# Optimization experiments

Hardware: AMD Instinct MI355X
Metric: run time of the kernel (lower is better)

Reference implementation:

```python
import jax, jax.numpy as jnp
import numpy as np

EPS = 1e-6  # F.pairwise_distance eps, added to each coordinate difference


def setup_inputs() -> dict:
    key = jax.random.key(0)
    x = jax.random.normal(key, (8192, 3, 192), dtype=jnp.float32)
    return {"x": x}


def reference(x):
    # x: [N, M, D]; positive = shot 0, anchor = mean of shots 1:
    anchor = jnp.mean(x[:, 1:, :], axis=1)          # [N, D]
    pos = x[:, 0, :]                                # [N, D]
    N, D = pos.shape

    # Legacy pairwise_distance reduces over D of the broadcast [N, D, N] diff:
    # dist2[i, j] = sum_d (pos[i,d] - anchor[j,d] + eps)^2
    # Expand exactly via GEMM to avoid materializing [N, D, N]:
    # = ||pos_i||^2 + ||anc_j||^2 - 2 pos_i.anc_j + 2*eps*(sum_d pos_i - sum_d anc_j) + D*eps^2
    pn = jnp.sum(pos * pos, axis=1)                 # [N]
    an = jnp.sum(anchor * anchor, axis=1)           # [N]
    cross = pos @ anchor.T                          # [N, N]
    sdiff = jnp.sum(pos, axis=1)[:, None] - jnp.sum(anchor, axis=1)[None, :]
    dist2 = pn[:, None] + an[None, :] - 2.0 * cross + 2.0 * EPS * sdiff + D * (EPS * EPS)
    output = -dist2                                 # [N, N] logits

    labels = jnp.arange(N)
    logp = jax.nn.log_softmax(output, axis=-1)
    nloss = -jnp.mean(jnp.take_along_axis(logp, labels[:, None], axis=1))

    pred = jnp.argmax(output, axis=1)               # top-1
    prec1 = jnp.mean((pred == labels).astype(jnp.float32)) * 100.0
    return (nloss, prec1)
```

## Files before the change

kernel.cpp:

```cpp
#include <hip/hip_runtime.h>
#include <math.h>


#define NROWS  8192
#define DDIM   192
#define KSPL   384
#define X3     576
#define FEPS   1e-6f
#define LOG2E  1.4426950408889634f
#define LN2    0.6931471805599453f

#define BM 128
#define BN 128
#define BK 64
#define KSTEPS 6
#define NSPLIT 8
#define JRANGE 1024
#define JTILES 8
#define NPART  16
#define NCOMB  32

typedef _Float16 f16;
typedef _Float16 f16x4 __attribute__((ext_vector_type(4)));
typedef _Float16 f16x8 __attribute__((ext_vector_type(8)));
typedef float    f32x4 __attribute__((ext_vector_type(4)));

__device__ __forceinline__ void async_copy16(const void* g, void* l) {
  __builtin_amdgcn_global_load_lds(
      (const __attribute__((address_space(1))) unsigned int*)g,
      (__attribute__((address_space(3))) unsigned int*)l, 16, 0, 0);
}

__global__ __launch_bounds__(256) void prep_kernel(const float* __restrict__ x,
                                                   f16* __restrict__ ph,
                                                   f16* __restrict__ ah,
                                                   float* __restrict__ bvec) {
  const int row  = (blockIdx.x * 256 + threadIdx.x) >> 6;
  const int lane = threadIdx.x & 63;
  float an = 0.f, as = 0.f;
  if (lane < 48) {
    const float* xr = x + (size_t)row * X3;
    const int d = lane * 4;
    const float4 p = *(const float4*)(xr + d);
    const float4 u = *(const float4*)(xr + DDIM + d);
    const float4 w = *(const float4*)(xr + 2 * DDIM + d);
    const float a0 = 0.5f * (u.x + w.x), a1 = 0.5f * (u.y + w.y);
    const float a2 = 0.5f * (u.z + w.z), a3 = 0.5f * (u.w + w.w);
    an = a0 * a0 + a1 * a1 + a2 * a2 + a3 * a3;
    as = a0 + a1 + a2 + a3;
    const float C2 = 2.0f * LOG2E;
    const float p0 = p.x * C2, p1 = p.y * C2, p2 = p.z * C2, p3 = p.w * C2;
    const f16 h0 = (f16)p0, h1 = (f16)p1, h2 = (f16)p2, h3 = (f16)p3;
    f16x4 hv = {h0, h1, h2, h3};
    f16x4 lv = {(f16)(p0 - (float)h0), (f16)(p1 - (float)h1),
                (f16)(p2 - (float)h2), (f16)(p3 - (float)h3)};
    *(f16x4*)(ph + (size_t)row * KSPL + d) = hv;
    *(f16x4*)(ph + (size_t)row * KSPL + DDIM + d) = lv;
    const f16 g0 = (f16)a0, g1 = (f16)a1, g2 = (f16)a2, g3 = (f16)a3;
    f16x4 gv = {g0, g1, g2, g3};
    f16x4 mv = {(f16)(a0 - (float)g0), (f16)(a1 - (float)g1),
                (f16)(a2 - (float)g2), (f16)(a3 - (float)g3)};
    *(f16x4*)(ah + (size_t)row * KSPL + d) = gv;
    *(f16x4*)(ah + (size_t)row * KSPL + DDIM + d) = mv;
  }
  #pragma unroll
  for (int m = 32; m; m >>= 1) {
    an += __shfl_xor(an, m);
    as += __shfl_xor(as, m);
  }
  if (lane == 0) bvec[row] = LOG2E * (-an + 2.0f * FEPS * as);
}

__global__ __launch_bounds__(256, 2) void main_kernel(
    const f16* __restrict__ Ag, const f16* __restrict__ Bg,
    const float* __restrict__ bvec,
    float* __restrict__ pm, float* __restrict__ ps, int* __restrict__ pa,
    float* __restrict__ diag) {
  __shared__ __align__(16) f16 As[2][BM * BK];
  __shared__ __align__(16) f16 Bs[2][BN * BK];
  const int tid  = threadIdx.x;
  const int lane = tid & 63;
  const int wid  = tid >> 6;
  const int wm = wid >> 1, wn = wid & 1;
  const int lLow = lane & 15, lHi = lane >> 4, l7 = lane & 7;
  const int i0 = blockIdx.x * BM;
  const int split = blockIdx.y;

  const int rsub = lane >> 3;
  const int srck = ((lane & 7) ^ rsub) * 8;

  auto stage = [&](int b, int jt, int kc) {
    const int j0 = split * JRANGE + jt * BN;
    #pragma unroll
    for (int q = 0; q < 4; ++q) {
      const int ci  = q * 4 + wid;
      const int row = ci * 8 + rsub;
      async_copy16(Ag + (size_t)(i0 + row) * KSPL + kc + srck, (void*)(&As[b][ci * 512]));
      async_copy16(Bg + (size_t)(j0 + row) * KSPL + kc + srck, (void*)(&Bs[b][ci * 512]));
    }
  };

  float mrun[16], srun[16];
  int   arun[16];
  #pragma unroll
  for (int r = 0; r < 16; ++r) { mrun[r] = -3.0e38f; srun[r] = 0.f; arun[r] = 0; }

  stage(0, 0, 0);
  __syncthreads();

  for (int jt = 0; jt < JTILES; ++jt) {
    f32x4 acc[4][4];
    #pragma unroll
    for (int mf = 0; mf < 4; ++mf)
      #pragma unroll
      for (int nf = 0; nf < 4; ++nf) acc[mf][nf] = (f32x4)0.f;

    #pragma unroll
    for (int ks = 0; ks < KSTEPS; ++ks) {
      if (!(jt == JTILES - 1 && ks == KSTEPS - 1)) {
        const int jn = (ks == KSTEPS - 1) ? jt + 1 : jt;
        const int kn = (ks == KSTEPS - 1) ? 0 : (ks + 1) * BK;
        stage((ks + 1) & 1, jn, kn);
      }
      const int b = ks & 1;
      #pragma unroll
      for (int kk = 0; kk < 2; ++kk) {
        const int ksw = ((kk * 4 + lHi) ^ l7) * 8;
        f16x8 af[4];
        #pragma unroll
        for (int mf = 0; mf < 4; ++mf)
          af[mf] = *(const f16x8*)(&As[b][(wm * 64 + mf * 16 + lLow) * 64 + ksw]);
        #pragma unroll
        for (int nf = 0; nf < 4; ++nf) {
          f16x8 bf = *(const f16x8*)(&Bs[b][(wn * 64 + nf * 16 + lLow) * 64 + ksw]);
          #pragma unroll
          for (int mf = 0; mf < 4; ++mf)
            acc[mf][nf] = __builtin_amdgcn_mfma_f32_16x16x32_f16(af[mf], bf, acc[mf][nf], 0, 0, 0);
        }
      }
      if (ks == KSTEPS - 1) {
        const int j0 = split * JRANGE + jt * BN;
        float bv[4];
        int   gc[4];
        #pragma unroll
        for (int nf = 0; nf < 4; ++nf) {
          gc[nf] = j0 + wn * 64 + nf * 16 + lLow;
          bv[nf] = bvec[gc[nf]];
        }
        const bool dtile = (split == (int)(blockIdx.x >> 3)) && (jt == (int)(blockIdx.x & 7));
        #pragma unroll
        for (int mf = 0; mf < 4; ++mf) {
          #pragma unroll
          for (int reg = 0; reg < 4; ++reg) {
            const int rs = mf * 4 + reg;
            const int grow = i0 + wm * 64 + mf * 16 + lHi * 4 + reg;
            float v0 = acc[mf][0][reg] + bv[0];
            float v1 = acc[mf][1][reg] + bv[1];
            float v2 = acc[mf][2][reg] + bv[2];
            float v3 = acc[mf][3][reg] + bv[3];
            if (dtile) {
              if (grow == gc[0]) diag[grow] = v0;
              if (grow == gc[1]) diag[grow] = v1;
              if (grow == gc[2]) diag[grow] = v2;
              if (grow == gc[3]) diag[grow] = v3;
            }
            float tm = v0; int tj = gc[0];
            if (v1 > tm) { tm = v1; tj = gc[1]; }
            if (v2 > tm) { tm = v2; tj = gc[2]; }
            if (v3 > tm) { tm = v3; tj = gc[3]; }
            float nm = fmaxf(tm, mrun[rs]);
            float se = exp2f(v0 - nm) + exp2f(v1 - nm) + exp2f(v2 - nm) + exp2f(v3 - nm);
            srun[rs] = srun[rs] * exp2f(mrun[rs] - nm) + se;
            if (tm > mrun[rs]) arun[rs] = tj;
            mrun[rs] = nm;
          }
        }
      }
      __syncthreads();
    }
  }

  #pragma unroll
  for (int rs = 0; rs < 16; ++rs) {
    float mm = mrun[rs], ss = srun[rs];
    int aa = arun[rs];
    #pragma unroll
    for (int d = 1; d < 16; d <<= 1) {
      float om = __shfl_xor(mm, d, 16);
      float os = __shfl_xor(ss, d, 16);
      int   oa = __shfl_xor(aa, d, 16);
      float nm = fmaxf(mm, om);
      ss = ss * exp2f(mm - nm) + os * exp2f(om - nm);
      if (om > mm || (om == mm && oa < aa)) aa = oa;
      mm = nm;
    }
    if (lLow == 0) {
      const int grow = i0 + wm * 64 + (rs >> 2) * 16 + lHi * 4 + (rs & 3);
      const int sidx = split * 2 + wn;
      pm[(size_t)sidx * NROWS + grow] = mm;
      ps[(size_t)sidx * NROWS + grow] = ss;
      pa[(size_t)sidx * NROWS + grow] = aa;
    }
  }
}

__global__ __launch_bounds__(256) void combine_partial(
    const float* __restrict__ pm, const float* __restrict__ ps,
    const int* __restrict__ pa, const float* __restrict__ diag,
    float* __restrict__ partL, float* __restrict__ partC) {
  const int i = blockIdx.x * 256 + threadIdx.x;
  float mm = pm[i];
  int   aa = pa[i];
  #pragma unroll
  for (int s = 1; s < NPART; ++s) {
    float om = pm[(size_t)s * NROWS + i];
    int   oa = pa[(size_t)s * NROWS + i];
    if (om > mm || (om == mm && oa < aa)) { mm = om; aa = oa; }
  }
  float ss = 0.f;
  #pragma unroll
  for (int s = 0; s < NPART; ++s)
    ss += ps[(size_t)s * NROWS + i] * exp2f(pm[(size_t)s * NROWS + i] - mm);
  float lsum = (mm + log2f(ss) - diag[i]) * LN2;
  float csum = (aa == i) ? 1.0f : 0.0f;
  #pragma unroll
  for (int d = 32; d; d >>= 1) {
    lsum += __shfl_xor(lsum, d);
    csum += __shfl_xor(csum, d);
  }
  __shared__ float wl[4], wc[4];
  int w = threadIdx.x >> 6;
  if ((threadIdx.x & 63) == 0) { wl[w] = lsum; wc[w] = csum; }
  __syncthreads();
  if (threadIdx.x == 0) {
    partL[blockIdx.x] = wl[0] + wl[1] + wl[2] + wl[3];
    partC[blockIdx.x] = wc[0] + wc[1] + wc[2] + wc[3];
  }
}

__global__ __launch_bounds__(64) void final_kernel(
    const float* __restrict__ partL, const float* __restrict__ partC,
    float* __restrict__ out) {
  int t = threadIdx.x;
  float l = (t < NCOMB) ? partL[t] : 0.f;
  float c = (t < NCOMB) ? partC[t] : 0.f;
  #pragma unroll
  for (int d = 32; d; d >>= 1) {
    l += __shfl_xor(l, d);
    c += __shfl_xor(c, d);
  }
  if (t == 0) {
    out[0] = l / (float)NROWS;
    out[1] = 100.f * c / (float)NROWS;
  }
}

extern "C" void kernel_launch(void* const* d_in, const int* in_sizes, int n_in,
                              void* d_out, int out_size, void* d_ws, size_t ws_size,
                              hipStream_t stream) {
  const float* x = (const float*)d_in[0];
  float* out = (float*)d_out;

  char* ws = (char*)d_ws;
  size_t off = 0;
  auto take = [&](size_t bytes) { void* p = ws + off; off += (bytes + 255) & ~(size_t)255; return p; };
  f16*   ph    = (f16*)take((size_t)NROWS * KSPL * sizeof(f16));
  f16*   ah    = (f16*)take((size_t)NROWS * KSPL * sizeof(f16));
  float* bvec  = (float*)take((size_t)NROWS * sizeof(float));
  float* pm    = (float*)take((size_t)NPART * NROWS * sizeof(float));
  float* ps    = (float*)take((size_t)NPART * NROWS * sizeof(float));
  int*   pa    = (int*)take((size_t)NPART * NROWS * sizeof(int));
  float* diag  = (float*)take((size_t)NROWS * sizeof(float));
  float* partL = (float*)take((size_t)NCOMB * sizeof(float));
  float* partC = (float*)take((size_t)NCOMB * sizeof(float));

  prep_kernel<<<dim3((NROWS * 64) / 256), 256, 0, stream>>>(x, ph, ah, bvec);
  main_kernel<<<dim3(NROWS / BM, NSPLIT), 256, 0, stream>>>(ph, ah, bvec, pm, ps, pa, diag);
  combine_partial<<<dim3(NCOMB), 256, 0, stream>>>(pm, ps, pa, diag, partL, partC);
  final_kernel<<<1, 64, 0, stream>>>(partL, partC, out);
}
```

Baseline: 186.2 us.

## Use 8-wave blocks with single-buffered LDS instead of double-buffered 4-wave pipeline

The main GEMM+softmax kernel goes from 256 to 512 threads per block. Each wave now owns a 32x64 sub-tile instead of 64x64, which halves the accumulator and running-softmax registers per thread and targets 4 blocks per CU through the launch bounds. The double-buffered asynchronous LDS prefetch is replaced by a single buffer that is loaded and then consumed between two barriers per k-step. This trades explicit load/compute overlap for more resident waves to hide latency, at the cost of extra synchronisation.

```diff
diff --git a/kernel.cpp b/kernel.cpp
--- a/kernel.cpp
+++ b/kernel.cpp
@@ -13,7 +13,6 @@
 #define BM 128
 #define BN 128
 #define BK 64
-#define KSTEPS 6
 #define NSPLIT 8
 #define JRANGE 1024
 #define JTILES 8
@@ -71,13 +70,13 @@
   if (lane == 0) bvec[row] = LOG2E * (-an + 2.0f * FEPS * as);
 }
 
-__global__ __launch_bounds__(256, 2) void main_kernel(
+__global__ __launch_bounds__(512, 4) void main_kernel(
     const f16* __restrict__ Ag, const f16* __restrict__ Bg,
     const float* __restrict__ bvec,
     float* __restrict__ pm, float* __restrict__ ps, int* __restrict__ pa,
     float* __restrict__ diag) {
-  __shared__ __align__(16) f16 As[2][BM * BK];
-  __shared__ __align__(16) f16 Bs[2][BN * BK];
+  __shared__ __align__(16) f16 As[BM * BK];
+  __shared__ __align__(16) f16 Bs[BN * BK];
   const int tid  = threadIdx.x;
   const int lane = tid & 63;
   const int wid  = tid >> 6;
@@ -87,101 +86,87 @@
   const int split = blockIdx.y;
 
   const int rsub = lane >> 3;
-  const int srck = ((lane & 7) ^ rsub) * 8;
-
-  auto stage = [&](int b, int jt, int kc) {
+  const int srck = (l7 ^ rsub) * 8;
+
+  float mrun[8], srun[8];
+  int   arun[8];
+  #pragma unroll
+  for (int r = 0; r < 8; ++r) { mrun[r] = -3.0e38f; srun[r] = 0.f; arun[r] = 0; }
+
+  for (int jt = 0; jt < JTILES; ++jt) {
     const int j0 = split * JRANGE + jt * BN;
-    #pragma unroll
-    for (int q = 0; q < 4; ++q) {
-      const int ci  = q * 4 + wid;
-      const int row = ci * 8 + rsub;
-      async_copy16(Ag + (size_t)(i0 + row) * KSPL + kc + srck, (void*)(&As[b][ci * 512]));
-      async_copy16(Bg + (size_t)(j0 + row) * KSPL + kc + srck, (void*)(&Bs[b][ci * 512]));
-    }
-  };
-
-  float mrun[16], srun[16];
-  int   arun[16];
-  #pragma unroll
-  for (int r = 0; r < 16; ++r) { mrun[r] = -3.0e38f; srun[r] = 0.f; arun[r] = 0; }
-
-  stage(0, 0, 0);
-  __syncthreads();
-
-  for (int jt = 0; jt < JTILES; ++jt) {
-    f32x4 acc[4][4];
-    #pragma unroll
-    for (int mf = 0; mf < 4; ++mf)
+    f32x4 acc[2][4];
+    #pragma unroll
+    for (int mf = 0; mf < 2; ++mf)
       #pragma unroll
       for (int nf = 0; nf < 4; ++nf) acc[mf][nf] = (f32x4)0.f;
 
-    #pragma unroll
-    for (int ks = 0; ks < KSTEPS; ++ks) {
-      if (!(jt == JTILES - 1 && ks == KSTEPS - 1)) {
-        const int jn = (ks == KSTEPS - 1) ? jt + 1 : jt;
-        const int kn = (ks == KSTEPS - 1) ? 0 : (ks + 1) * BK;
-        stage((ks + 1) & 1, jn, kn);
+    for (int kc = 0; kc < KSPL; kc += BK) {
+      __syncthreads();
+      #pragma unroll
+      for (int q = 0; q < 2; ++q) {
+        const int ci  = q * 8 + wid;
+        const int row = ci * 8 + rsub;
+        async_copy16(Ag + (size_t)(i0 + row) * KSPL + kc + srck, (void*)(As + ci * 512));
+        async_copy16(Bg + (size_t)(j0 + row) * KSPL + kc + srck, (void*)(Bs + ci * 512));
       }
-      const int b = ks & 1;
+      __syncthreads();
       #pragma unroll
       for (int kk = 0; kk < 2; ++kk) {
         const int ksw = ((kk * 4 + lHi) ^ l7) * 8;
-        f16x8 af[4];
+        f16x8 af[2];
         #pragma unroll
-        for (int mf = 0; mf < 4; ++mf)
-          af[mf] = *(const f16x8*)(&As[b][(wm * 64 + mf * 16 + lLow) * 64 + ksw]);
+        for (int mf = 0; mf < 2; ++mf)
+          af[mf] = *(const f16x8*)(As + (wm * 32 + mf * 16 + lLow) * 64 + ksw);
         #pragma unroll
         for (int nf = 0; nf < 4; ++nf) {
-          f16x8 bf = *(const f16x8*)(&Bs[b][(wn * 64 + nf * 16 + lLow) * 64 + ksw]);
+          f16x8 bf = *(const f16x8*)(Bs + (wn * 64 + nf * 16 + lLow) * 64 + ksw);
           #pragma unroll
-          for (int mf = 0; mf < 4; ++mf)
+          for (int mf = 0; mf < 2; ++mf)
             acc[mf][nf] = __builtin_amdgcn_mfma_f32_16x16x32_f16(af[mf], bf, acc[mf][nf], 0, 0, 0);
         }
       }
-      if (ks == KSTEPS - 1) {
-        const int j0 = split * JRANGE + jt * BN;
-        float bv[4];
-        int   gc[4];
-        #pragma unroll
-        for (int nf = 0; nf < 4; ++nf) {
-          gc[nf] = j0 + wn * 64 + nf * 16 + lLow;
-          bv[nf] = bvec[gc[nf]];
+    }
+
+    float bv[4];
+    int   gc[4];
+    #pragma unroll
+    for (int nf = 0; nf < 4; ++nf) {
+      gc[nf] = j0 + wn * 64 + nf * 16 + lLow;
+      bv[nf] = bvec[gc[nf]];
+    }
+    const bool dtile = (split == (int)(blockIdx.x >> 3)) && (jt == (int)(blockIdx.x & 7));
+    #pragma unroll
+    for (int mf = 0; mf < 2; ++mf) {
+      #pragma unroll
+      for (int reg = 0; reg < 4; ++reg) {
+        const int rs = mf * 4 + reg;
+        const int grow = i0 + wm * 32 + mf * 16 + lHi * 4 + reg;
+        float v0 = acc[mf][0][reg] + bv[0];
+        float v1 = acc[mf][1][reg] + bv[1];
+        float v2 = acc[mf][2][reg] + bv[2];
+        float v3 = acc[mf][3][reg] + bv[3];
+        if (dtile) {
+          if (grow == gc[0]) diag[grow] = v0;
+          if (grow == gc[1]) diag[grow] = v1;
+          if (grow == gc[2]) diag[grow] = v2;
+          if (grow == gc[3]) diag[grow] = v3;
         }
-        const bool dtile = (split == (int)(blockIdx.x >> 3)) && (jt == (int)(blockIdx.x & 7));
-        #pragma unroll
-        for (int mf = 0; mf < 4; ++mf) {
-          #pragma unroll
-          for (int reg = 0; reg < 4; ++reg) {
-            const int rs = mf * 4 + reg;
-            const int grow = i0 + wm * 64 + mf * 16 + lHi * 4 + reg;
-            float v0 = acc[mf][0][reg] + bv[0];
-            float v1 = acc[mf][1][reg] + bv[1];
-            float v2 = acc[mf][2][reg] + bv[2];
-            float v3 = acc[mf][3][reg] + bv[3];
-            if (dtile) {
-              if (grow == gc[0]) diag[grow] = v0;
-              if (grow == gc[1]) diag[grow] = v1;
-              if (grow == gc[2]) diag[grow] = v2;
-              if (grow == gc[3]) diag[grow] = v3;
-            }
-            float tm = v0; int tj = gc[0];
-            if (v1 > tm) { tm = v1; tj = gc[1]; }
-            if (v2 > tm) { tm = v2; tj = gc[2]; }
-            if (v3 > tm) { tm = v3; tj = gc[3]; }
-            float nm = fmaxf(tm, mrun[rs]);
-            float se = exp2f(v0 - nm) + exp2f(v1 - nm) + exp2f(v2 - nm) + exp2f(v3 - nm);
-            srun[rs] = srun[rs] * exp2f(mrun[rs] - nm) + se;
-            if (tm > mrun[rs]) arun[rs] = tj;
-            mrun[rs] = nm;
-          }
-        }
+        float tm = v0; int tj = gc[0];
+        if (v1 > tm) { tm = v1; tj = gc[1]; }
+        if (v2 > tm) { tm = v2; tj = gc[2]; }
+        if (v3 > tm) { tm = v3; tj = gc[3]; }
+        float nm = fmaxf(tm, mrun[rs]);
+        float se = exp2f(v0 - nm) + exp2f(v1 - nm) + exp2f(v2 - nm) + exp2f(v3 - nm);
+        srun[rs] = srun[rs] * exp2f(mrun[rs] - nm) + se;
+        if (tm > mrun[rs]) arun[rs] = tj;
+        mrun[rs] = nm;
       }
-      __syncthreads();
-    }
-  }
-
-  #pragma unroll
-  for (int rs = 0; rs < 16; ++rs) {
+    }
+  }
+
+  #pragma unroll
+  for (int rs = 0; rs < 8; ++rs) {
     float mm = mrun[rs], ss = srun[rs];
     int aa = arun[rs];
     #pragma unroll
@@ -195,7 +180,7 @@
       mm = nm;
     }
     if (lLow == 0) {
-      const int grow = i0 + wm * 64 + (rs >> 2) * 16 + lHi * 4 + (rs & 3);
+      const int grow = i0 + wm * 32 + (rs >> 2) * 16 + lHi * 4 + (rs & 3);
       const int sidx = split * 2 + wn;
       pm[(size_t)sidx * NROWS + grow] = mm;
       ps[(size_t)sidx * NROWS + grow] = ss;
@@ -275,7 +260,7 @@
   float* partC = (float*)take((size_t)NCOMB * sizeof(float));
 
   prep_kernel<<<dim3((NROWS * 64) / 256), 256, 0, stream>>>(x, ph, ah, bvec);
-  main_kernel<<<dim3(NROWS / BM, NSPLIT), 256, 0, stream>>>(ph, ah, bvec, pm, ps, pa, diag);
+  main_kernel<<<dim3(NROWS / BM, NSPLIT), 512, 0, stream>>>(ph, ah, bvec, pm, ps, pa, diag);
   combine_partial<<<dim3(NCOMB), 256, 0, stream>>>(pm, ps, pa, diag, partL, partC);
   final_kernel<<<1, 64, 0, stream>>>(partL, partC, out);
 }
```

Measured after the change: 174.9 us. -6.1%, faster.

## Replace syncthreads with fenceless barriers and explicit vmcnt waits in GEMM pipeline

Applied to the files above, without the earlier changes.

Replaces __syncthreads in the double-buffered main loop with raw s_barrier calls plus explicit s_waitcnt vmcnt counts. The next stage's async copies can then stay in flight while the current buffer is consumed, instead of draining every outstanding load at each barrier. The bvec loads and the next tile's staging are issued before the last k-step's MFMAs. The risk is subtle race bugs if the vmcnt counts do not match the number of outstanding global-to-LDS loads, and there are now two barriers per step instead of one.

```diff
diff --git a/kernel.cpp b/kernel.cpp
--- a/kernel.cpp
+++ b/kernel.cpp
@@ -29,6 +29,12 @@
   __builtin_amdgcn_global_load_lds(
       (const __attribute__((address_space(1))) unsigned int*)g,
       (__attribute__((address_space(3))) unsigned int*)l, 16, 0, 0);
+}
+
+__device__ __forceinline__ void barrier_nofence_drain() {
+  asm volatile("" ::: "memory");
+  __builtin_amdgcn_s_barrier();
+  asm volatile("" ::: "memory");
 }
 
 __global__ __launch_bounds__(256) void prep_kernel(const float* __restrict__ x,
@@ -87,7 +93,7 @@
   const int split = blockIdx.y;
 
   const int rsub = lane >> 3;
-  const int srck = ((lane & 7) ^ rsub) * 8;
+  const int srck = (l7 ^ rsub) * 8;
 
   auto stage = [&](int b, int jt, int kc) {
     const int j0 = split * JRANGE + jt * BN;
@@ -106,8 +112,8 @@
   for (int r = 0; r < 16; ++r) { mrun[r] = -3.0e38f; srun[r] = 0.f; arun[r] = 0; }
 
   stage(0, 0, 0);
-  __syncthreads();
-
+
+  int p = 0;
   for (int jt = 0; jt < JTILES; ++jt) {
     f32x4 acc[4][4];
     #pragma unroll
@@ -117,28 +123,28 @@
 
     #pragma unroll
     for (int ks = 0; ks < KSTEPS; ++ks) {
-      if (!(jt == JTILES - 1 && ks == KSTEPS - 1)) {
-        const int jn = (ks == KSTEPS - 1) ? jt + 1 : jt;
-        const int kn = (ks == KSTEPS - 1) ? 0 : (ks + 1) * BK;
-        stage((ks + 1) & 1, jn, kn);
-      }
-      const int b = ks & 1;
-      #pragma unroll
-      for (int kk = 0; kk < 2; ++kk) {
-        const int ksw = ((kk * 4 + lHi) ^ l7) * 8;
-        f16x8 af[4];
+      barrier_nofence_drain();
+
+      if (ks < KSTEPS - 1) {
+        stage(p ^ 1, jt, (ks + 1) * BK);
+        asm volatile("s_waitcnt vmcnt(8)" ::: "memory");
+        barrier_nofence_drain();
         #pragma unroll
-        for (int mf = 0; mf < 4; ++mf)
-          af[mf] = *(const f16x8*)(&As[b][(wm * 64 + mf * 16 + lLow) * 64 + ksw]);
-        #pragma unroll
-        for (int nf = 0; nf < 4; ++nf) {
-          f16x8 bf = *(const f16x8*)(&Bs[b][(wn * 64 + nf * 16 + lLow) * 64 + ksw]);
+        for (int kk = 0; kk < 2; ++kk) {
+          const int ksw = ((kk * 4 + lHi) ^ l7) * 8;
+          f16x8 af[4];
           #pragma unroll
           for (int mf = 0; mf < 4; ++mf)
-            acc[mf][nf] = __builtin_amdgcn_mfma_f32_16x16x32_f16(af[mf], bf, acc[mf][nf], 0, 0, 0);
-        }
-      }
-      if (ks == KSTEPS - 1) {
+            af[mf] = *(const f16x8*)(&As[p][(wm * 64 + mf * 16 + lLow) * 64 + ksw]);
+          #pragma unroll
+          for (int nf = 0; nf < 4; ++nf) {
+            f16x8 bf = *(const f16x8*)(&Bs[p][(wn * 64 + nf * 16 + lLow) * 64 + ksw]);
+            #pragma unroll
+            for (int mf = 0; mf < 4; ++mf)
+              acc[mf][nf] = __builtin_amdgcn_mfma_f32_16x16x32_f16(af[mf], bf, acc[mf][nf], 0, 0, 0);
+          }
+        }
+      } else {
         const int j0 = split * JRANGE + jt * BN;
         float bv[4];
         int   gc[4];
@@ -146,6 +152,28 @@
         for (int nf = 0; nf < 4; ++nf) {
           gc[nf] = j0 + wn * 64 + nf * 16 + lLow;
           bv[nf] = bvec[gc[nf]];
+        }
+        if (jt < JTILES - 1) {
+          stage(p ^ 1, jt + 1, 0);
+          asm volatile("s_waitcnt vmcnt(12)" ::: "memory");
+        } else {
+          asm volatile("s_waitcnt vmcnt(4)" ::: "memory");
+        }
+        barrier_nofence_drain();
+        #pragma unroll
+        for (int kk = 0; kk < 2; ++kk) {
+          const int ksw = ((kk * 4 + lHi) ^ l7) * 8;
+          f16x8 af[4];
+          #pragma unroll
+          for (int mf = 0; mf < 4; ++mf)
+            af[mf] = *(const f16x8*)(&As[p][(wm * 64 + mf * 16 + lLow) * 64 + ksw]);
+          #pragma unroll
+          for (int nf = 0; nf < 4; ++nf) {
+            f16x8 bf = *(const f16x8*)(&Bs[p][(wn * 64 + nf * 16 + lLow) * 64 + ksw]);
+            #pragma unroll
+            for (int mf = 0; mf < 4; ++mf)
+              acc[mf][nf] = __builtin_amdgcn_mfma_f32_16x16x32_f16(af[mf], bf, acc[mf][nf], 0, 0, 0);
+          }
         }
         const bool dtile = (split == (int)(blockIdx.x >> 3)) && (jt == (int)(blockIdx.x & 7));
         #pragma unroll
@@ -176,7 +204,7 @@
           }
         }
       }
-      __syncthreads();
+      p ^= 1;
     }
   }
 
```

Result: faster. 168.9 us (-9.3%).

## Drop fp16 split-precision terms, halve K, raise occupancy, single-buffer LDS

Applied to the files above, without the earlier changes.

Removes the hi/lo fp16 split of the positive and anchor vectors, so the GEMM reduction dimension is cut from 384 to 192 and the MFMA work and operand traffic halve. The LDS tiles go from double- to single-buffered with explicit barriers around each load. The column split doubles to 16 and launch bounds target 4 blocks per CU, relying on occupancy instead of software pipelining to hide load latency. Plain fp16 operands lower the accuracy of the logits, which could flip argmax ties or shift the loss beyond tolerance.

```diff
diff --git a/kernel.cpp b/kernel.cpp
--- a/kernel.cpp
+++ b/kernel.cpp
@@ -4,7 +4,7 @@
 
 #define NROWS  8192
 #define DDIM   192
-#define KSPL   384
+#define KSPL   192
 #define X3     576
 #define FEPS   1e-6f
 #define LOG2E  1.4426950408889634f
@@ -13,11 +13,10 @@
 #define BM 128
 #define BN 128
 #define BK 64
-#define KSTEPS 6
-#define NSPLIT 8
-#define JRANGE 1024
-#define JTILES 8
-#define NPART  16
+#define NSPLIT 16
+#define JRANGE 512
+#define JTILES 4
+#define NPART  32
 #define NCOMB  32
 
 typedef _Float16 f16;
@@ -49,19 +48,10 @@
     an = a0 * a0 + a1 * a1 + a2 * a2 + a3 * a3;
     as = a0 + a1 + a2 + a3;
     const float C2 = 2.0f * LOG2E;
-    const float p0 = p.x * C2, p1 = p.y * C2, p2 = p.z * C2, p3 = p.w * C2;
-    const f16 h0 = (f16)p0, h1 = (f16)p1, h2 = (f16)p2, h3 = (f16)p3;
-    f16x4 hv = {h0, h1, h2, h3};
-    f16x4 lv = {(f16)(p0 - (float)h0), (f16)(p1 - (float)h1),
-                (f16)(p2 - (float)h2), (f16)(p3 - (float)h3)};
+    f16x4 hv = {(f16)(p.x * C2), (f16)(p.y * C2), (f16)(p.z * C2), (f16)(p.w * C2)};
     *(f16x4*)(ph + (size_t)row * KSPL + d) = hv;
-    *(f16x4*)(ph + (size_t)row * KSPL + DDIM + d) = lv;
-    const f16 g0 = (f16)a0, g1 = (f16)a1, g2 = (f16)a2, g3 = (f16)a3;
-    f16x4 gv = {g0, g1, g2, g3};
-    f16x4 mv = {(f16)(a0 - (float)g0), (f16)(a1 - (float)g1),
-                (f16)(a2 - (float)g2), (f16)(a3 - (float)g3)};
+    f16x4 gv = {(f16)a0, (f16)a1, (f16)a2, (f16)a3};
     *(f16x4*)(ah + (size_t)row * KSPL + d) = gv;
-    *(f16x4*)(ah + (size_t)row * KSPL + DDIM + d) = mv;
   }
   #pragma unroll
   for (int m = 32; m; m >>= 1) {
@@ -71,13 +61,13 @@
   if (lane == 0) bvec[row] = LOG2E * (-an + 2.0f * FEPS * as);
 }
 
-__global__ __launch_bounds__(256, 2) void main_kernel(
+__global__ __launch_bounds__(256, 4) void main_kernel(
     const f16* __restrict__ Ag, const f16* __restrict__ Bg,
     const float* __restrict__ bvec,
     float* __restrict__ pm, float* __restrict__ ps, int* __restrict__ pa,
     float* __restrict__ diag) {
-  __shared__ __align__(16) f16 As[2][BM * BK];
-  __shared__ __align__(16) f16 Bs[2][BN * BK];
+  __shared__ __align__(16) f16 As[BM * BK];
+  __shared__ __align__(16) f16 Bs[BN * BK];
   const int tid  = threadIdx.x;
   const int lane = tid & 63;
   const int wid  = tid >> 6;
@@ -87,28 +77,15 @@
   const int split = blockIdx.y;
 
   const int rsub = lane >> 3;
-  const int srck = ((lane & 7) ^ rsub) * 8;
-
-  auto stage = [&](int b, int jt, int kc) {
-    const int j0 = split * JRANGE + jt * BN;
-    #pragma unroll
-    for (int q = 0; q < 4; ++q) {
-      const int ci  = q * 4 + wid;
-      const int row = ci * 8 + rsub;
-      async_copy16(Ag + (size_t)(i0 + row) * KSPL + kc + srck, (void*)(&As[b][ci * 512]));
-      async_copy16(Bg + (size_t)(j0 + row) * KSPL + kc + srck, (void*)(&Bs[b][ci * 512]));
-    }
-  };
+  const int srck = (l7 ^ rsub) * 8;
 
   float mrun[16], srun[16];
   int   arun[16];
   #pragma unroll
   for (int r = 0; r < 16; ++r) { mrun[r] = -3.0e38f; srun[r] = 0.f; arun[r] = 0; }
 
-  stage(0, 0, 0);
-  __syncthreads();
-
   for (int jt = 0; jt < JTILES; ++jt) {
+    const int j0 = split * JRANGE + jt * BN;
     f32x4 acc[4][4];
     #pragma unroll
     for (int mf = 0; mf < 4; ++mf)
@@ -116,67 +93,67 @@
       for (int nf = 0; nf < 4; ++nf) acc[mf][nf] = (f32x4)0.f;
 
     #pragma unroll
-    for (int ks = 0; ks < KSTEPS; ++ks) {
-      if (!(jt == JTILES - 1 && ks == KSTEPS - 1)) {
-        const int jn = (ks == KSTEPS - 1) ? jt + 1 : jt;
-        const int kn = (ks == KSTEPS - 1) ? 0 : (ks + 1) * BK;
-        stage((ks + 1) & 1, jn, kn);
+    for (int kc = 0; kc < KSPL; kc += BK) {
+      __syncthreads();
+      #pragma unroll
+      for (int q = 0; q < 4; ++q) {
+        const int ci  = q * 4 + wid;
+        const int row = ci * 8 + rsub;
+        async_copy16(Ag + (size_t)(i0 + row) * KSPL + kc + srck, (void*)(As + ci * 512));
+        async_copy16(Bg + (size_t)(j0 + row) * KSPL + kc + srck, (void*)(Bs + ci * 512));
       }
-      const int b = ks & 1;
+      __syncthreads();
       #pragma unroll
       for (int kk = 0; kk < 2; ++kk) {
         const int ksw = ((kk * 4 + lHi) ^ l7) * 8;
         f16x8 af[4];
         #pragma unroll
         for (int mf = 0; mf < 4; ++mf)
-          af[mf] = *(const f16x8*)(&As[b][(wm * 64 + mf * 16 + lLow) * 64 + ksw]);
+          af[mf] = *(const f16x8*)(As + (wm * 64 + mf * 16 + lLow) * 64 + ksw);
         #pragma unroll
         for (int nf = 0; nf < 4; ++nf) {
-          f16x8 bf = *(const f16x8*)(&Bs[b][(wn * 64 + nf * 16 + lLow) * 64 + ksw]);
+          f16x8 bf = *(const f16x8*)(Bs + (wn * 64 + nf * 16 + lLow) * 64 + ksw);
           #pragma unroll
           for (int mf = 0; mf < 4; ++mf)
             acc[mf][nf] = __builtin_amdgcn_mfma_f32_16x16x32_f16(af[mf], bf, acc[mf][nf], 0, 0, 0);
         }
       }
-      if (ks == KSTEPS - 1) {
-        const int j0 = split * JRANGE + jt * BN;
-        float bv[4];
-        int   gc[4];
-        #pragma unroll
-        for (int nf = 0; nf < 4; ++nf) {
-          gc[nf] = j0 + wn * 64 + nf * 16 + lLow;
-          bv[nf] = bvec[gc[nf]];
+    }
+
+    float bv[4];
+    int   gc[4];
+    #pragma unroll
+    for (int nf = 0; nf < 4; ++nf) {
+      gc[nf] = j0 + wn * 64 + nf * 16 + lLow;
+      bv[nf] = bvec[gc[nf]];
+    }
+    const bool dtile = (split == (int)(blockIdx.x >> 2)) && (jt == (int)(blockIdx.x & 3));
+    #pragma unroll
+    for (int mf = 0; mf < 4; ++mf) {
+      #pragma unroll
+      for (int reg = 0; reg < 4; ++reg) {
+        const int rs = mf * 4 + reg;
+        const int grow = i0 + wm * 64 + mf * 16 + lHi * 4 + reg;
+        float v0 = acc[mf][0][reg] + bv[0];
+        float v1 = acc[mf][1][reg] + bv[1];
+        float v2 = acc[mf][2][reg] + bv[2];
+        float v3 = acc[mf][3][reg] + bv[3];
+        if (dtile) {
+          if (grow == gc[0]) diag[grow] = v0;
+          if (grow == gc[1]) diag[grow] = v1;
+          if (grow == gc[2]) diag[grow] = v2;
+          if (grow == gc[3]) diag[grow] = v3;
         }
-        const bool dtile = (split == (int)(blockIdx.x >> 3)) && (jt == (int)(blockIdx.x & 7));
-        #pragma unroll
-        for (int mf = 0; mf < 4; ++mf) {
-          #pragma unroll
-          for (int reg = 0; reg < 4; ++reg) {
-            const int rs = mf * 4 + reg;
-            const int grow = i0 + wm * 64 + mf * 16 + lHi * 4 + reg;
-            float v0 = acc[mf][0][reg] + bv[0];
-            float v1 = acc[mf][1][reg] + bv[1];
-            float v2 = acc[mf][2][reg] + bv[2];
-            float v3 = acc[mf][3][reg] + bv[3];
-            if (dtile) {
-              if (grow == gc[0]) diag[grow] = v0;
-              if (grow == gc[1]) diag[grow] = v1;
-              if (grow == gc[2]) diag[grow] = v2;
-              if (grow == gc[3]) diag[grow] = v3;
-            }
-            float tm = v0; int tj = gc[0];
-            if (v1 > tm) { tm = v1; tj = gc[1]; }
-            if (v2 > tm) { tm = v2; tj = gc[2]; }
-            if (v3 > tm) { tm = v3; tj = gc[3]; }
-            float nm = fmaxf(tm, mrun[rs]);
-            float se = exp2f(v0 - nm) + exp2f(v1 - nm) + exp2f(v2 - nm) + exp2f(v3 - nm);
-            srun[rs] = srun[rs] * exp2f(mrun[rs] - nm) + se;
-            if (tm > mrun[rs]) arun[rs] = tj;
-            mrun[rs] = nm;
-          }
-        }
+        float tm = v0; int tj = gc[0];
+        if (v1 > tm) { tm = v1; tj = gc[1]; }
+        if (v2 > tm) { tm = v2; tj = gc[2]; }
+        if (v3 > tm) { tm = v3; tj = gc[3]; }
+        float nm = fmaxf(tm, mrun[rs]);
+        float se = exp2f(v0 - nm) + exp2f(v1 - nm) + exp2f(v2 - nm) + exp2f(v3 - nm);
+        srun[rs] = srun[rs] * exp2f(mrun[rs] - nm) + se;
+        if (tm > mrun[rs]) arun[rs] = tj;
+        mrun[rs] = nm;
       }
-      __syncthreads();
     }
   }
 
```

Result: slower. 236.4 us (+27.0%).
